# Kernel optimization log

Measured on AMD Instinct MI355X. Metric: run time of the kernel, lower is better.

## Reference

```python
import jax, jax.numpy as jnp
import numpy as np

K = 10        # neighbors kept (after dropping self)
N_SEEDS = 20  # FPS seeds
H = 0.01      # repulsion bandwidth


def setup_inputs() -> dict:
    key = jax.random.key(0)
    pcs = jax.random.uniform(key, (16, 65536, 3), dtype=jnp.float32)
    return {"pcs": pcs}


def farthest_point_sample(xyz, npoint, key):
    """Iterative FPS. xyz: [B,N,C] -> centroids [B,npoint] (int)."""
    B, N, C = xyz.shape
    distance = jnp.full((B, N), 1e10, dtype=xyz.dtype)
    farthest = jax.random.randint(key, (B,), 0, N)
    bidx = jnp.arange(B)

    def step(carry, _):
        dist_min, far = carry
        centroid = xyz[bidx, far][:, None, :]              # [B,1,C]
        d = jnp.sum((xyz - centroid) ** 2, axis=-1)        # [B,N]
        dist_min = jnp.minimum(dist_min, d)
        return (dist_min, jnp.argmax(dist_min, axis=-1)), far

    _, cents = jax.lax.scan(step, (distance, farthest), None, length=npoint)
    return cents.T  # [B, npoint]


def reference(pcs):
    B, N, C = pcs.shape
    seeds = farthest_point_sample(pcs, N_SEEDS, jax.random.key(1))   # [B,S]
    seeds_value = jnp.take_along_axis(
        pcs, jnp.broadcast_to(seeds[:, :, None], (B, N_SEEDS, C)), axis=1
    )  # [B,S,3]
    diff = pcs[:, :, None, :] - seeds_value[:, None, :, :]           # [B,N,S,3]
    sq = jnp.sum(diff * diff, axis=-1)                               # [B,N,S]
    # safe L2 norm (exact zeros at seed-vs-itself)
    dist = jnp.where(sq == 0, 0.0, jnp.sqrt(jnp.where(sq == 0, 1.0, sq)))
    dist_sn = dist.transpose(0, 2, 1)                                # [B,S,N]
    # k+1 smallest distances per seed, ascending (torch.topk largest=False)
    neg_top, _ = jax.lax.top_k(-dist_sn, K + 1)                      # [B,S,K+1]
    top_dist_net = -neg_top[:, :, 1:]                                # drop self, [B,S,K]
    weights = jnp.exp(-(top_dist_net ** 2) / (H * H))
    repulsion = -top_dist_net * weights
    return repulsion.sum(axis=2).sum(axis=1).mean()
```

## Files before the change

### kernel.cpp

```cpp
#include <hip/hip_runtime.h>
#include <cstdint>
#include <cfloat>
#include <cmath>

#define NPTS 65536
#define NB 16
#define NS 20
#define KK 10
#define FPB 16
#define NSm1 (NS - 1)

struct InitIdx { int idx[NB]; };

static __device__ __forceinline__ unsigned long long
agent_ld(const unsigned long long* p) {
    return __hip_atomic_load(p, __ATOMIC_RELAXED, __HIP_MEMORY_SCOPE_AGENT);
}

__global__ __launch_bounds__(1024) void fps_kernel(const float* __restrict__ pcs,
                                                   int* __restrict__ seeds,
                                                   unsigned long long* __restrict__ fkey,
                                                   InitIdx init) {
    const int u   = blockIdx.x;
    const int xcd = u & 7;
    const int k   = u >> 3;
    const int b   = 2 * xcd + (k >> 4);
    const int j   = k & 15;
    const int t   = threadIdx.x;
    const int lane = t & 63;
    const int w    = t >> 6;
    const float* __restrict__ base = pcs + (size_t)b * NPTS * 3;
    const int pbase = j * 4096 + t * 4;

    const float4* q4 = reinterpret_cast<const float4*>(base + (size_t)pbase * 3);
    float4 A = q4[0], Bv = q4[1], Cv = q4[2];
    float x[4] = { A.x, A.w, Bv.z, Cv.y };
    float y[4] = { A.y, Bv.x, Bv.w, Cv.z };
    float z[4] = { A.z, Bv.y, Cv.x, Cv.w };
    float dm[4] = { 1e10f, 1e10f, 1e10f, 1e10f };

    __shared__ float s_val[16];
    __shared__ int   s_idx[16];
    __shared__ int   s_far;

    int far = init.idx[b];

    for (int s = 0; s < NS; ++s) {
        if (j == 0 && t == 0) seeds[b * NS + s] = far;
        if (s == NSm1) break;

        const float* c = base + (size_t)far * 3;
        const float cx = c[0], cy = c[1], cz = c[2];

        float bestv = -1.0f;
        int   besti = 0;
#pragma unroll
        for (int q = 0; q < 4; ++q) {
            float dx = __fsub_rn(x[q], cx);
            float dy = __fsub_rn(y[q], cy);
            float dz = __fsub_rn(z[q], cz);
            float d  = __fadd_rn(__fadd_rn(__fmul_rn(dx, dx), __fmul_rn(dy, dy)),
                                 __fmul_rn(dz, dz));
            dm[q] = fminf(dm[q], d);
            if (dm[q] > bestv) { bestv = dm[q]; besti = pbase + q; }
        }
#pragma unroll
        for (int off = 32; off >= 1; off >>= 1) {
            float ov = __shfl_down(bestv, off);
            int   oi = __shfl_down(besti, off);
            if (ov > bestv || (ov == bestv && oi < besti)) { bestv = ov; besti = oi; }
        }
        if (lane == 0) { s_val[w] = bestv; s_idx[w] = besti; }
        __syncthreads();

        if (w == 0) {
            unsigned long long kv = 0ULL;
            if (lane < 16) {
                kv = ((unsigned long long)__float_as_uint(s_val[lane]) << 32) |
                     (unsigned long long)(0xFFFFFFFFu - (unsigned int)s_idx[lane]);
            }
#pragma unroll
            for (int off = 8; off >= 1; off >>= 1) {
                unsigned int lo = (unsigned int)kv, hi = (unsigned int)(kv >> 32);
                unsigned int olo = (unsigned int)__shfl_xor((int)lo, off);
                unsigned int ohi = (unsigned int)__shfl_xor((int)hi, off);
                unsigned long long o = ((unsigned long long)ohi << 32) | olo;
                if (o > kv) kv = o;
            }
            unsigned long long* fp = fkey + (size_t)(b * NS + s) * FPB;
            if (lane == 0)
                __hip_atomic_store(&fp[j], kv, __ATOMIC_RELAXED,
                                   __HIP_MEMORY_SCOPE_AGENT);

            const unsigned long long* sl = fp + (lane & 15);
            unsigned long long p0 = agent_ld(sl);
            unsigned long long p1 = agent_ld(sl);
            unsigned long long p2 = agent_ld(sl);
            unsigned long long v;
            for (;;) {
                if (!__any(p0 == 0ULL)) { v = p0; break; }
                p0 = agent_ld(sl);
                if (!__any(p1 == 0ULL)) { v = p1; break; }
                p1 = agent_ld(sl);
                if (!__any(p2 == 0ULL)) { v = p2; break; }
                p2 = agent_ld(sl);
            }
#pragma unroll
            for (int off = 32; off >= 1; off >>= 1) {
                unsigned int lo = (unsigned int)v, hi = (unsigned int)(v >> 32);
                unsigned int olo = (unsigned int)__shfl_xor((int)lo, off);
                unsigned int ohi = (unsigned int)__shfl_xor((int)hi, off);
                unsigned long long o = ((unsigned long long)ohi << 32) | olo;
                if (o > v) v = o;
            }
            if (lane == 0)
                s_far = (int)(0xFFFFFFFFu - (unsigned int)(v & 0xFFFFFFFFull));
        }
        __syncthreads();
        far = s_far;
    }
}

__global__ __launch_bounds__(1024) void knn_kernel(const float* __restrict__ pcs,
                                                   const int* __restrict__ seeds,
                                                   float* __restrict__ out) {
    const int u   = blockIdx.x;
    const int xcd = u & 7;
    const int k   = u >> 3;
    const int b   = 2 * xcd + (k & 1);
    const int s   = k >> 1;
    const int t = threadIdx.x;
    const int lane = t & 63;
    const int w = t >> 6;
    const float* __restrict__ base = pcs + (size_t)b * NPTS * 3;
    const int sidx = seeds[b * NS + s];
    const float cx = base[(size_t)sidx * 3 + 0];
    const float cy = base[(size_t)sidx * 3 + 1];
    const float cz = base[(size_t)sidx * 3 + 2];

    float lst[11];
#pragma unroll
    for (int jj = 0; jj < 11; ++jj) lst[jj] = FLT_MAX;

    for (int i = 0; i < 16; ++i) {
        const int pbase = i * 4096 + t * 4;
        const float4* q4 = reinterpret_cast<const float4*>(base + (size_t)pbase * 3);
        float4 A = q4[0], Bv = q4[1], Cv = q4[2];
        float px[4] = { A.x, A.w, Bv.z, Cv.y };
        float py[4] = { A.y, Bv.x, Bv.w, Cv.z };
        float pz[4] = { A.z, Bv.y, Cv.x, Cv.w };
#pragma unroll
        for (int q = 0; q < 4; ++q) {
            float dx = __fsub_rn(px[q], cx);
            float dy = __fsub_rn(py[q], cy);
            float dz = __fsub_rn(pz[q], cz);
            float sq = __fadd_rn(__fadd_rn(__fmul_rn(dx, dx), __fmul_rn(dy, dy)),
                                 __fmul_rn(dz, dz));
#pragma unroll
            for (int jj = 10; jj >= 1; --jj)
                lst[jj] = __builtin_amdgcn_fmed3f(lst[jj - 1], lst[jj], sq);
            lst[0] = fminf(lst[0], sq);
        }
    }

    __shared__ float s_top[16][11];
    for (int r = 0; r < 11; ++r) {
        float v = lst[0];
#pragma unroll
        for (int off = 32; off >= 1; off >>= 1) v = fminf(v, __shfl_xor(v, off));
        unsigned long long m = __ballot(lst[0] == v);
        if (lane == (int)__ffsll(m) - 1) {
#pragma unroll
            for (int jj = 0; jj < 10; ++jj) lst[jj] = lst[jj + 1];
            lst[10] = FLT_MAX;
        }
        if (lane == 0) s_top[w][r] = v;
    }
    __syncthreads();

    if (w == 0) {
        const float* flat = &s_top[0][0];
        float a0 = flat[lane];
        float a1 = flat[lane + 64];
        float a2 = (lane + 128 < 176) ? flat[lane + 128] : FLT_MAX;

        const float HH = (float)(0.01 * 0.01);
        float acc = 0.0f;
#pragma unroll
        for (int r = 0; r < 11; ++r) {
            float mymin = fminf(a0, fminf(a1, a2));
            float v = mymin;
#pragma unroll
            for (int off = 32; off >= 1; off >>= 1) v = fminf(v, __shfl_xor(v, off));
            unsigned long long m = __ballot(mymin == v);
            if (lane == (int)__ffsll(m) - 1) {
                if (a0 == v)      a0 = FLT_MAX;
                else if (a1 == v) a1 = FLT_MAX;
                else              a2 = FLT_MAX;
            }
            if (lane == 0 && r >= 1) {
                float sq = v;
                float d  = (sq == 0.0f) ? 0.0f : __fsqrt_rn(sq);
                float q2 = __fmul_rn(d, d);
                float wt = expf(__fdiv_rn(-q2, HH));
                acc = __fadd_rn(acc, -__fmul_rn(d, wt));
            }
        }
        if (lane == 0) atomicAdd(out, acc * 0.0625f);
    }
}

static inline uint32_t rotl32(uint32_t x, uint32_t d) { return (x << d) | (x >> (32 - d)); }

static void tf2x32(uint32_t k0, uint32_t k1, uint32_t x0, uint32_t x1,
                   uint32_t& y0, uint32_t& y1) {
    const uint32_t ks[3] = { k0, k1, k0 ^ k1 ^ 0x1BD11BDAu };
    const uint32_t rotA[4] = { 13, 15, 26, 6 };
    const uint32_t rotB[4] = { 17, 29, 16, 24 };
    uint32_t v0 = x0 + ks[0], v1 = x1 + ks[1];
    for (int i = 0; i < 5; ++i) {
        const uint32_t* rot = (i % 2 == 0) ? rotA : rotB;
        for (int j = 0; j < 4; ++j) {
            v0 += v1;
            v1 = rotl32(v1, rot[j]);
            v1 ^= v0;
        }
        v0 += ks[(i + 1) % 3];
        v1 += ks[(i + 2) % 3] + (uint32_t)(i + 1);
    }
    y0 = v0; y1 = v1;
}

extern "C" void kernel_launch(void* const* d_in, const int* in_sizes, int n_in,
                              void* d_out, int out_size, void* d_ws, size_t ws_size,
                              hipStream_t stream) {
    const float* pcs = (const float*)d_in[0];
    float* out = (float*)d_out;

    int* seeds               = (int*)d_ws;
    unsigned long long* fkey = (unsigned long long*)((char*)d_ws + 2048);

    uint32_t k2_0, k2_1;
    tf2x32(0u, 1u, 0u, 1u, k2_0, k2_1);
    InitIdx init;
    for (int i = 0; i < NB; ++i) {
        uint32_t y0, y1;
        tf2x32(k2_0, k2_1, 0u, (uint32_t)i, y0, y1);
        init.idx[i] = (int)((y0 ^ y1) & 0xFFFFu);
    }

    hipMemsetAsync(d_ws, 0, 43008, stream);
    hipMemsetAsync(d_out, 0, sizeof(float), stream);

    hipLaunchKernelGGL(fps_kernel, dim3(NB * FPB), dim3(1024), 0, stream,
                       pcs, seeds, fkey, init);
    hipLaunchKernelGGL(knn_kernel, dim3(NB * NS), dim3(1024), 0, stream,
                       pcs, seeds, out);
}
```

Measured before the change: 82.35 us.

## Fuse kNN scan into FPS kernel with per-slice partial top-k and small merge kernel

The kNN distance scan moves into the tail of the FPS kernel. Each of the 16 blocks per batch already covers a 4096-point slice, and each wave now scans that slice for one or two seeds, writing an 11-element partial top-k to workspace. A small 64-thread merge kernel then combines the 16 partial lists per (batch, seed) and computes the repulsion term. This reuses the FPS grid and the cache-resident slice instead of launching a separate kernel that rereads the whole cloud per seed. The cost is serial work at the end of FPS, uneven load because waves 0-3 handle two seeds, and an extra launch plus a global round trip for the partials.

New measurement: 77.11 us. -6.4%, faster.

```diff
diff --git a/kernel.cpp b/kernel.cpp
--- a/kernel.cpp
+++ b/kernel.cpp
@@ -17,10 +17,33 @@
     return __hip_atomic_load(p, __ATOMIC_RELAXED, __HIP_MEMORY_SCOPE_AGENT);
 }
 
-__global__ __launch_bounds__(1024) void fps_kernel(const float* __restrict__ pcs,
-                                                   int* __restrict__ seeds,
-                                                   unsigned long long* __restrict__ fkey,
-                                                   InitIdx init) {
+#define INS11(L, SQ)                                                     \
+    {                                                                    \
+        _Pragma("unroll")                                                \
+        for (int jj = 10; jj >= 1; --jj)                                 \
+            L[jj] = __builtin_amdgcn_fmed3f(L[jj - 1], L[jj], (SQ));     \
+        L[0] = fminf(L[0], (SQ));                                        \
+    }
+
+#define WAVEPOP11(L, DEST)                                               \
+    for (int r = 0; r < 11; ++r) {                                       \
+        float v = L[0];                                                  \
+        _Pragma("unroll")                                                \
+        for (int off = 32; off >= 1; off >>= 1)                          \
+            v = fminf(v, __shfl_xor(v, off));                            \
+        unsigned long long m = __ballot(L[0] == v);                      \
+        if (lane == (int)__ffsll(m) - 1) {                               \
+            _Pragma("unroll")                                            \
+            for (int jj = 0; jj < 10; ++jj) L[jj] = L[jj + 1];           \
+            L[10] = FLT_MAX;                                             \
+        }                                                                \
+        if (lane == 0) (DEST)[r] = v;                                    \
+    }
+
+__global__ __launch_bounds__(1024, 4) void fps_kernel(const float* __restrict__ pcs,
+                                                      unsigned long long* __restrict__ fkey,
+                                                      float* __restrict__ part,
+                                                      InitIdx init) {
     const int u   = blockIdx.x;
     const int xcd = u & 7;
     const int k   = u >> 3;
@@ -42,11 +65,12 @@
     __shared__ float s_val[16];
     __shared__ int   s_idx[16];
     __shared__ int   s_far;
+    __shared__ int   s_seeds[NS];
 
     int far = init.idx[b];
 
     for (int s = 0; s < NS; ++s) {
-        if (j == 0 && t == 0) seeds[b * NS + s] = far;
+        if (t == 0) s_seeds[s] = far;
         if (s == NSm1) break;
 
         const float* c = base + (size_t)far * 3;
@@ -119,95 +143,75 @@
         __syncthreads();
         far = s_far;
     }
-}
-
-__global__ __launch_bounds__(1024) void knn_kernel(const float* __restrict__ pcs,
-                                                   const int* __restrict__ seeds,
-                                                   float* __restrict__ out) {
-    const int u   = blockIdx.x;
-    const int xcd = u & 7;
-    const int k   = u >> 3;
-    const int b   = 2 * xcd + (k & 1);
-    const int s   = k >> 1;
-    const int t = threadIdx.x;
-    const int lane = t & 63;
-    const int w = t >> 6;
-    const float* __restrict__ base = pcs + (size_t)b * NPTS * 3;
-    const int sidx = seeds[b * NS + s];
-    const float cx = base[(size_t)sidx * 3 + 0];
-    const float cy = base[(size_t)sidx * 3 + 1];
-    const float cz = base[(size_t)sidx * 3 + 2];
-
-    float lst[11];
-#pragma unroll
-    for (int jj = 0; jj < 11; ++jj) lst[jj] = FLT_MAX;
-
-    for (int i = 0; i < 16; ++i) {
-        const int pbase = i * 4096 + t * 4;
-        const float4* q4 = reinterpret_cast<const float4*>(base + (size_t)pbase * 3);
-        float4 A = q4[0], Bv = q4[1], Cv = q4[2];
-        float px[4] = { A.x, A.w, Bv.z, Cv.y };
-        float py[4] = { A.y, Bv.x, Bv.w, Cv.z };
-        float pz[4] = { A.z, Bv.y, Cv.x, Cv.w };
-#pragma unroll
-        for (int q = 0; q < 4; ++q) {
-            float dx = __fsub_rn(px[q], cx);
-            float dy = __fsub_rn(py[q], cy);
-            float dz = __fsub_rn(pz[q], cz);
-            float sq = __fadd_rn(__fadd_rn(__fmul_rn(dx, dx), __fmul_rn(dy, dy)),
-                                 __fmul_rn(dz, dz));
-#pragma unroll
-            for (int jj = 10; jj >= 1; --jj)
-                lst[jj] = __builtin_amdgcn_fmed3f(lst[jj - 1], lst[jj], sq);
-            lst[0] = fminf(lst[0], sq);
-        }
-    }
-
-    __shared__ float s_top[16][11];
+
+    __syncthreads();
+#pragma unroll
+    for (int pass = 0; pass < 2; ++pass) {
+        const int s2 = w + pass * 16;
+        if (s2 >= NS) break;
+        const int sidx = s_seeds[s2];
+        const float ccx = base[(size_t)sidx * 3 + 0];
+        const float ccy = base[(size_t)sidx * 3 + 1];
+        const float ccz = base[(size_t)sidx * 3 + 2];
+
+        float lst[11];
+#pragma unroll
+        for (int jj = 0; jj < 11; ++jj) lst[jj] = FLT_MAX;
+
+        for (int i = 0; i < 16; ++i) {
+            const int pt = j * 4096 + (i * 64 + lane) * 4;
+            const float4* qq = reinterpret_cast<const float4*>(base + (size_t)pt * 3);
+            float4 qa = qq[0], qb = qq[1], qc = qq[2];
+            float px[4] = { qa.x, qa.w, qb.z, qc.y };
+            float py[4] = { qa.y, qb.x, qb.w, qc.z };
+            float pz[4] = { qa.z, qb.y, qc.x, qc.w };
+#pragma unroll
+            for (int q = 0; q < 4; ++q) {
+                float dx = __fsub_rn(px[q], ccx);
+                float dy = __fsub_rn(py[q], ccy);
+                float dz = __fsub_rn(pz[q], ccz);
+                float sq = __fadd_rn(__fadd_rn(__fmul_rn(dx, dx), __fmul_rn(dy, dy)),
+                                     __fmul_rn(dz, dz));
+                INS11(lst, sq);
+            }
+        }
+        float* pr = part + ((size_t)(b * NS + s2) * FPB + j) * 11;
+        WAVEPOP11(lst, pr);
+    }
+}
+
+__global__ __launch_bounds__(64) void knn_merge(const float* __restrict__ part,
+                                               float* __restrict__ out) {
+    const int pair = blockIdx.x;
+    const int lane = threadIdx.x;
+    const float* flat = part + (size_t)pair * 176;
+    float a0 = flat[lane];
+    float a1 = flat[lane + 64];
+    float a2 = (lane + 128 < 176) ? flat[lane + 128] : FLT_MAX;
+
+    const float HH = (float)(0.01 * 0.01);
+    float acc = 0.0f;
+#pragma unroll
     for (int r = 0; r < 11; ++r) {
-        float v = lst[0];
+        float mymin = fminf(a0, fminf(a1, a2));
+        float v = mymin;
 #pragma unroll
         for (int off = 32; off >= 1; off >>= 1) v = fminf(v, __shfl_xor(v, off));
-        unsigned long long m = __ballot(lst[0] == v);
+        unsigned long long m = __ballot(mymin == v);
         if (lane == (int)__ffsll(m) - 1) {
-#pragma unroll
-            for (int jj = 0; jj < 10; ++jj) lst[jj] = lst[jj + 1];
-            lst[10] = FLT_MAX;
-        }
-        if (lane == 0) s_top[w][r] = v;
-    }
-    __syncthreads();
-
-    if (w == 0) {
-        const float* flat = &s_top[0][0];
-        float a0 = flat[lane];
-        float a1 = flat[lane + 64];
-        float a2 = (lane + 128 < 176) ? flat[lane + 128] : FLT_MAX;
-
-        const float HH = (float)(0.01 * 0.01);
-        float acc = 0.0f;
-#pragma unroll
-        for (int r = 0; r < 11; ++r) {
-            float mymin = fminf(a0, fminf(a1, a2));
-            float v = mymin;
-#pragma unroll
-            for (int off = 32; off >= 1; off >>= 1) v = fminf(v, __shfl_xor(v, off));
-            unsigned long long m = __ballot(mymin == v);
-            if (lane == (int)__ffsll(m) - 1) {
-                if (a0 == v)      a0 = FLT_MAX;
-                else if (a1 == v) a1 = FLT_MAX;
-                else              a2 = FLT_MAX;
-            }
-            if (lane == 0 && r >= 1) {
-                float sq = v;
-                float d  = (sq == 0.0f) ? 0.0f : __fsqrt_rn(sq);
-                float q2 = __fmul_rn(d, d);
-                float wt = expf(__fdiv_rn(-q2, HH));
-                acc = __fadd_rn(acc, -__fmul_rn(d, wt));
-            }
-        }
-        if (lane == 0) atomicAdd(out, acc * 0.0625f);
-    }
+            if (a0 == v)      a0 = FLT_MAX;
+            else if (a1 == v) a1 = FLT_MAX;
+            else              a2 = FLT_MAX;
+        }
+        if (lane == 0 && r >= 1) {
+            float sq = v;
+            float d  = (sq == 0.0f) ? 0.0f : __fsqrt_rn(sq);
+            float q2 = __fmul_rn(d, d);
+            float wt = expf(__fdiv_rn(-q2, HH));
+            acc = __fadd_rn(acc, -__fmul_rn(d, wt));
+        }
+    }
+    if (lane == 0) atomicAdd(out, acc * 0.0625f);
 }
 
 static inline uint32_t rotl32(uint32_t x, uint32_t d) { return (x << d) | (x >> (32 - d)); }
@@ -237,8 +241,8 @@
     const float* pcs = (const float*)d_in[0];
     float* out = (float*)d_out;
 
-    int* seeds               = (int*)d_ws;
     unsigned long long* fkey = (unsigned long long*)((char*)d_ws + 2048);
+    float* part              = (float*)((char*)d_ws + 49152);
 
     uint32_t k2_0, k2_1;
     tf2x32(0u, 1u, 0u, 1u, k2_0, k2_1);
@@ -249,11 +253,11 @@
         init.idx[i] = (int)((y0 ^ y1) & 0xFFFFu);
     }
 
-    hipMemsetAsync(d_ws, 0, 43008, stream);
+    hipMemsetAsync((char*)d_ws + 2048, 0, 40960, stream);
     hipMemsetAsync(d_out, 0, sizeof(float), stream);
 
     hipLaunchKernelGGL(fps_kernel, dim3(NB * FPB), dim3(1024), 0, stream,
-                       pcs, seeds, fkey, init);
-    hipLaunchKernelGGL(knn_kernel, dim3(NB * NS), dim3(1024), 0, stream,
-                       pcs, seeds, out);
-}
+                       pcs, fkey, part, init);
+    hipLaunchKernelGGL(knn_merge, dim3(320), dim3(64), 0, stream,
+                       part, out);
+}
```
